# Kernel optimization log

Measured on AMD Instinct MI355X. Metric: run time of the kernel, lower is better.

The kernel has to match this reference:

```python
import jax, jax.numpy as jnp
import numpy as np

EMB_DIM = 1024
HEAD = 16
HEAD_DIM = EMB_DIM // HEAD


def setup_inputs() -> dict:
    key = jax.random.key(0)
    ks = jax.random.split(key, 6)
    s = 1.0 / np.sqrt(EMB_DIM)
    return {
        "z": jax.random.normal(ks[0], (4, 2048, EMB_DIM), dtype=jnp.float32),
        "w_q": jax.random.normal(ks[1], (EMB_DIM, EMB_DIM), dtype=jnp.float32) * s,
        "w_k": jax.random.normal(ks[2], (EMB_DIM, EMB_DIM), dtype=jnp.float32) * s,
        "w_v": jax.random.normal(ks[3], (EMB_DIM, EMB_DIM), dtype=jnp.float32) * s,
        "w_o": jax.random.normal(ks[4], (EMB_DIM, EMB_DIM), dtype=jnp.float32) * s,
        "b_o": jax.random.normal(ks[5], (EMB_DIM,), dtype=jnp.float32) * 0.01,
    }


def reference(z, w_q, w_k, w_v, w_o, b_o):
    B, N, D = z.shape
    # QKV projections (nn.Linear: x @ W.T; here weights stored as (D_in, D_out))
    q = (z @ w_q).reshape(B, N, HEAD, HEAD_DIM).transpose(0, 2, 1, 3)  # bhnd
    k = (z @ w_k).reshape(B, N, HEAD, HEAD_DIM).transpose(0, 2, 1, 3)
    v = (z @ w_v).reshape(B, N, HEAD, HEAD_DIM).transpose(0, 2, 1, 3)
    scale = 1.0 / np.sqrt(HEAD_DIM).astype(np.float32)
    dots = jnp.einsum("bhnd,bhmd->bhnm", q, k) * scale
    attn = jax.nn.softmax(dots, axis=-1)
    out = jnp.einsum("bhnm,bhmd->bhnd", attn, v)
    out = out.transpose(0, 2, 1, 3).reshape(B, N, D)
    return out @ w_o + b_o
```

## Files before the change

### kernel.cpp

```cpp
#include <hip/hip_runtime.h>
#include <hip/hip_bf16.h>
#include <stdint.h>

typedef unsigned short u16;
typedef __attribute__((ext_vector_type(8))) short bf16x8;
typedef __attribute__((ext_vector_type(4))) float f32x4;
typedef __attribute__((ext_vector_type(16))) float f32x16;

static __device__ inline u16 f2bf(float f) {
  union { float f; uint32_t u; } v; v.f = f;
  uint32_t u = v.u;
  u += 0x7fffu + ((u >> 16) & 1);
  return (u16)(u >> 16);
}

static __device__ inline float fast_exp2(float x) {
#if __has_builtin(__builtin_amdgcn_exp2f)
  return __builtin_amdgcn_exp2f(x);
#else
  return __expf(x * 0.6931471805599453f);
#endif
}

static __device__ inline uint32_t pack_bf16(float lo, float hi) {
#if __has_builtin(__builtin_amdgcn_cvt_pk_bf16_f32)
  typedef __attribute__((ext_vector_type(2))) __bf16 bf16x2_t;
  bf16x2_t r = __builtin_amdgcn_cvt_pk_bf16_f32(lo, hi);
  union { bf16x2_t v; uint32_t u; } c; c.v = r;
  return c.u;
#else
  union { float f; uint32_t u; } a, b;
  a.f = lo; b.f = hi;
  uint32_t ua = a.u + 0x8000u;
  uint32_t ub = b.u + 0x8000u;
  return __builtin_amdgcn_perm(ub, ua, 0x07060302u);
#endif
}

__global__ __launch_bounds__(256) void cast_bf16_kernel(const float* __restrict__ src,
                                                        u16* __restrict__ dst, int n4) {
  int i = blockIdx.x * 256 + threadIdx.x;
  if (i < n4) {
    float4 v = reinterpret_cast<const float4*>(src)[i];
    uint2 o;
    o.x = (uint32_t)f2bf(v.x) | ((uint32_t)f2bf(v.y) << 16);
    o.y = (uint32_t)f2bf(v.z) | ((uint32_t)f2bf(v.w) << 16);
    reinterpret_cast<uint2*>(dst)[i] = o;
  }
}

__global__ __launch_bounds__(256) void wtrans_kernel(const float* __restrict__ wq,
                                                     const float* __restrict__ wk,
                                                     const float* __restrict__ wv,
                                                     const float* __restrict__ wo,
                                                     u16* __restrict__ bqkv,
                                                     u16* __restrict__ wot) {
  int z = blockIdx.z;
  const float* src = (z == 0) ? wq : (z == 1) ? wk : (z == 2) ? wv : wo;
  u16* dst = (z < 3) ? (bqkv + (size_t)z * 1024 * 1024) : wot;
  __shared__ float tile[32][33];
  int c0 = blockIdx.x * 32, r0 = blockIdx.y * 32;
  int tx = threadIdx.x, ty = threadIdx.y;
#pragma unroll
  for (int i = 0; i < 32; i += 8)
    tile[ty + i][tx] = src[(size_t)(r0 + ty + i) * 1024 + c0 + tx];
  __syncthreads();
#pragma unroll
  for (int i = 0; i < 32; i += 8)
    dst[(size_t)(c0 + ty + i) * 1024 + r0 + tx] = f2bf(tile[tx][ty + i]);
}

template <int MODE>
__global__ __launch_bounds__(256) void gemm_bt_kernel(
    const u16* __restrict__ A, const u16* __restrict__ Bt,
    u16* __restrict__ outQ, u16* __restrict__ outK, u16* __restrict__ outVt,
    float* __restrict__ outC, const float* __restrict__ bias) {
  const int Kd = 1024;
  const int n0 = blockIdx.x * 128;
  const int m0 = blockIdx.y * 128;
  __shared__ __align__(16) u16 Asm[128 * 40];
  __shared__ __align__(16) u16 Bsm[128 * 40];
  const int tid = threadIdx.x;
  const int wave = tid >> 6, lane = tid & 63;
  const int quad = lane >> 4, l15 = lane & 15;
  const int wm = (wave >> 1) * 64, wn = (wave & 1) * 64;
  const int srow = tid >> 2, spart = tid & 3;

  f32x4 acc[4][4] = {};

  for (int k0 = 0; k0 < Kd; k0 += 32) {
    __syncthreads();
    uint4 a0 = *reinterpret_cast<const uint4*>(A + (size_t)(m0 + srow) * Kd + k0 + spart * 8);
    uint4 a1 = *reinterpret_cast<const uint4*>(A + (size_t)(m0 + srow + 64) * Kd + k0 + spart * 8);
    uint4 b0 = *reinterpret_cast<const uint4*>(Bt + (size_t)(n0 + srow) * Kd + k0 + spart * 8);
    uint4 b1 = *reinterpret_cast<const uint4*>(Bt + (size_t)(n0 + srow + 64) * Kd + k0 + spart * 8);
    *reinterpret_cast<uint4*>(Asm + srow * 40 + spart * 8) = a0;
    *reinterpret_cast<uint4*>(Asm + (srow + 64) * 40 + spart * 8) = a1;
    *reinterpret_cast<uint4*>(Bsm + srow * 40 + spart * 8) = b0;
    *reinterpret_cast<uint4*>(Bsm + (srow + 64) * 40 + spart * 8) = b1;
    __syncthreads();
    bf16x8 af[4], bf[4];
#pragma unroll
    for (int i = 0; i < 4; i++)
      af[i] = *reinterpret_cast<const bf16x8*>(Asm + (wm + i * 16 + l15) * 40 + quad * 8);
#pragma unroll
    for (int i = 0; i < 4; i++)
      bf[i] = *reinterpret_cast<const bf16x8*>(Bsm + (wn + i * 16 + l15) * 40 + quad * 8);
#pragma unroll
    for (int mi = 0; mi < 4; mi++)
#pragma unroll
      for (int ni = 0; ni < 4; ni++)
        acc[mi][ni] = __builtin_amdgcn_mfma_f32_16x16x32_bf16(af[mi], bf[ni], acc[mi][ni], 0, 0, 0);
  }

  if (MODE == 0) {
    const int which = (n0 + wn) >> 10;
#pragma unroll
    for (int mi = 0; mi < 4; mi++)
#pragma unroll
      for (int ni = 0; ni < 4; ni++) {
        int n = n0 + wn + ni * 16 + l15;
        int hn = n & 1023;
        int h = hn >> 6, dim = hn & 63;
        if (which == 2) {
          int m = m0 + wm + mi * 16 + quad * 4;
          int b = m >> 11, tok = m & 2047;
          uint2 pk;
          pk.x = pack_bf16(acc[mi][ni][0], acc[mi][ni][1]);
          pk.y = pack_bf16(acc[mi][ni][2], acc[mi][ni][3]);
          *reinterpret_cast<uint2*>(outVt + ((size_t)(b * 16 + h) * 64 + dim) * 2048 + tok) = pk;
        } else {
          u16* dst = (which == 0) ? outQ : outK;
          float qscale = (which == 0) ? 0.1803368801111204f : 1.0f;
#pragma unroll
          for (int r = 0; r < 4; r++) {
            int m = m0 + wm + mi * 16 + quad * 4 + r;
            int b = m >> 11, tok = m & 2047;
            dst[(((size_t)(b * 16 + h)) * 2048 + tok) * 64 + dim] = f2bf(acc[mi][ni][r] * qscale);
          }
        }
      }
  } else {
#pragma unroll
    for (int mi = 0; mi < 4; mi++)
#pragma unroll
      for (int ni = 0; ni < 4; ni++) {
        int n = n0 + wn + ni * 16 + l15;
        float bv = bias[n];
#pragma unroll
        for (int r = 0; r < 4; r++) {
          int m = m0 + wm + mi * 16 + quad * 4 + r;
          outC[(size_t)m * 1024 + n] = acc[mi][ni][r] + bv;
        }
      }
  }
}

__global__ __launch_bounds__(256, 4) void attn_kernel(const u16* __restrict__ Q,
                                                      const u16* __restrict__ K,
                                                      const u16* __restrict__ Vt,
                                                      u16* __restrict__ Oout) {
  const int bh = blockIdx.y;
  const int q0 = blockIdx.x * 128;
  const int tid = threadIdx.x;
  const int wave = tid >> 6, lane = tid & 63;
  const int l31 = lane & 31, h = lane >> 5;

  __shared__ __align__(16) u16 QPs[128 * 72];
  __shared__ __align__(16) u16 Ks[64 * 72];
  __shared__ __align__(16) u16 Vs[64 * 72];

  const u16* Qg = Q + ((size_t)bh * 2048 + q0) * 64;
  const u16* Kg = K + (size_t)bh * 2048 * 64;
  const u16* Vg = Vt + (size_t)bh * 64 * 2048;

#pragma unroll
  for (int k = 0; k < 4; k++) {
    int c = tid + k * 256;
    int row = c >> 3, col = (c & 7) * 8;
    *reinterpret_cast<uint4*>(&QPs[row * 72 + col]) =
        *reinterpret_cast<const uint4*>(Qg + row * 64 + col);
  }
  __syncthreads();
  bf16x8 qf[4];
#pragma unroll
  for (int dc = 0; dc < 4; dc++)
    qf[dc] = *reinterpret_cast<const bf16x8*>(&QPs[(wave * 32 + l31) * 72 + dc * 16 + h * 8]);

  u16* Pw = &QPs[wave * 32 * 72];
  float ls0 = 0.f, ls1 = 0.f, ls2 = 0.f, ls3 = 0.f;
  f32x16 oacc[2] = {};

  for (int kt = 0; kt < 2048; kt += 64) {
    __syncthreads();
#pragma unroll
    for (int k = 0; k < 2; k++) {
      int c = tid + k * 256;
      int row = c >> 3, col = (c & 7) * 8;
      *reinterpret_cast<uint4*>(&Ks[row * 72 + col]) =
          *reinterpret_cast<const uint4*>(Kg + (size_t)(kt + row) * 64 + col);
      *reinterpret_cast<uint4*>(&Vs[row * 72 + col]) =
          *reinterpret_cast<const uint4*>(Vg + (size_t)row * 2048 + kt + col);
    }
    __syncthreads();

#pragma unroll
    for (int kb = 0; kb < 2; kb++) {
      f32x16 s = {};
#pragma unroll
      for (int dc = 0; dc < 4; dc++) {
        bf16x8 kf = *reinterpret_cast<const bf16x8*>(&Ks[(kb * 32 + l31) * 72 + dc * 16 + h * 8]);
        s = __builtin_amdgcn_mfma_f32_32x32x16_bf16(kf, qf[dc], s, 0, 0, 0);
      }
      float p[16];
#pragma unroll
      for (int i = 0; i < 16; i++) p[i] = fast_exp2(s[i]);
#pragma unroll
      for (int i = 0; i < 16; i += 4) {
        ls0 += p[i]; ls1 += p[i + 1]; ls2 += p[i + 2]; ls3 += p[i + 3];
      }
#pragma unroll
      for (int rg = 0; rg < 4; rg++) {
        uint2 pk;
        pk.x = pack_bf16(p[rg * 4 + 0], p[rg * 4 + 1]);
        pk.y = pack_bf16(p[rg * 4 + 2], p[rg * 4 + 3]);
        *reinterpret_cast<uint2*>(&Pw[l31 * 72 + kb * 32 + rg * 8 + h * 4]) = pk;
      }
    }

    bf16x8 pf[4];
#pragma unroll
    for (int kc = 0; kc < 4; kc++)
      pf[kc] = *reinterpret_cast<const bf16x8*>(&Pw[l31 * 72 + kc * 16 + h * 8]);
#pragma unroll
    for (int dt = 0; dt < 2; dt++) {
#pragma unroll
      for (int kc = 0; kc < 4; kc++) {
        bf16x8 vf = *reinterpret_cast<const bf16x8*>(&Vs[(dt * 32 + l31) * 72 + kc * 16 + h * 8]);
        oacc[dt] = __builtin_amdgcn_mfma_f32_32x32x16_bf16(pf[kc], vf, oacc[dt], 0, 0, 0);
      }
    }
  }

  float lsum = (ls0 + ls1) + (ls2 + ls3);
  lsum += __shfl_xor(lsum, 32, 64);
  float inv[16];
#pragma unroll
  for (int reg = 0; reg < 16; reg++) {
    int qq = (reg & 3) + 8 * (reg >> 2) + 4 * h;
    int lv = __builtin_amdgcn_ds_bpermute(qq << 2, __float_as_int(lsum));
    inv[reg] = __builtin_amdgcn_rcpf(__int_as_float(lv));
  }

  const int b = bh >> 4, hd = bh & 15;
  u16* dst = Oout + (size_t)b * 2048 * 1024 + (size_t)hd * 64;
#pragma unroll
  for (int dt = 0; dt < 2; dt++)
#pragma unroll
    for (int reg = 0; reg < 16; reg++) {
      int qq = q0 + wave * 32 + (reg & 3) + 8 * (reg >> 2) + 4 * h;
      dst[(size_t)qq * 1024 + dt * 32 + l31] = f2bf(oacc[dt][reg] * inv[reg]);
    }
}

extern "C" void kernel_launch(void* const* d_in, const int* in_sizes, int n_in,
                              void* d_out, int out_size, void* d_ws, size_t ws_size,
                              hipStream_t stream) {
  (void)in_sizes; (void)n_in; (void)out_size; (void)ws_size;
  const float* z  = (const float*)d_in[0];
  const float* wq = (const float*)d_in[1];
  const float* wk = (const float*)d_in[2];
  const float* wv = (const float*)d_in[3];
  const float* wo = (const float*)d_in[4];
  const float* bo = (const float*)d_in[5];
  float* out = (float*)d_out;

  char* ws = (char*)d_ws;
  u16* zb   = (u16*)(ws);
  u16* bqkv = (u16*)(ws + (16ull << 20));
  u16* wot  = (u16*)(ws + (22ull << 20));
  u16* Qb   = (u16*)(ws + (24ull << 20));
  u16* Kb   = (u16*)(ws + (40ull << 20));
  u16* Vtb  = (u16*)(ws + (56ull << 20));
  u16* Ob   = zb;

  cast_bf16_kernel<<<8192, 256, 0, stream>>>(z, zb, 2097152);
  wtrans_kernel<<<dim3(32, 32, 4), dim3(32, 8), 0, stream>>>(wq, wk, wv, wo, bqkv, wot);
  gemm_bt_kernel<0><<<dim3(24, 64), 256, 0, stream>>>(zb, bqkv, Qb, Kb, Vtb, nullptr, nullptr);
  attn_kernel<<<dim3(16, 64), 256, 0, stream>>>(Qb, Kb, Vtb, Ob);
  gemm_bt_kernel<1><<<dim3(8, 64), 256, 0, stream>>>(Ob, wot, nullptr, nullptr, nullptr, out, bo);
}
```

Before: 308.1 us.

## Prefetch K/V tiles in registers, use direct global-to-LDS loads in GEMM

The attention kernel now loads the next K/V tile into registers while the current tile is being computed, then writes it to shared memory after a barrier. This hides global load latency behind the QK and PV MFMA work. The GEMM staging loads switch to global_load_lds with an unpadded 32-wide LDS layout, which may bring back bank conflicts on fragment reads. The attention grid is also swapped so that blocks sharing the same head launch apart, and the cast kernel now uses the packed bf16 conversion.

```diff
diff --git a/kernel.cpp b/kernel.cpp
--- a/kernel.cpp
+++ b/kernel.cpp
@@ -37,14 +37,20 @@
 #endif
 }
 
+static __device__ __forceinline__ void load_lds_128(const u16* g, u16* l) {
+  __builtin_amdgcn_global_load_lds((const __attribute__((address_space(1))) void*)g,
+                                   (__attribute__((address_space(3))) void*)l,
+                                   16, 0, 0);
+}
+
 __global__ __launch_bounds__(256) void cast_bf16_kernel(const float* __restrict__ src,
                                                         u16* __restrict__ dst, int n4) {
   int i = blockIdx.x * 256 + threadIdx.x;
   if (i < n4) {
     float4 v = reinterpret_cast<const float4*>(src)[i];
     uint2 o;
-    o.x = (uint32_t)f2bf(v.x) | ((uint32_t)f2bf(v.y) << 16);
-    o.y = (uint32_t)f2bf(v.z) | ((uint32_t)f2bf(v.w) << 16);
+    o.x = pack_bf16(v.x, v.y);
+    o.y = pack_bf16(v.z, v.w);
     reinterpret_cast<uint2*>(dst)[i] = o;
   }
 }
@@ -78,34 +84,37 @@
   const int Kd = 1024;
   const int n0 = blockIdx.x * 128;
   const int m0 = blockIdx.y * 128;
-  __shared__ __align__(16) u16 Asm[128 * 40];
-  __shared__ __align__(16) u16 Bsm[128 * 40];
+  __shared__ __align__(16) u16 Asm[128 * 32];
+  __shared__ __align__(16) u16 Bsm[128 * 32];
   const int tid = threadIdx.x;
   const int wave = tid >> 6, lane = tid & 63;
   const int quad = lane >> 4, l15 = lane & 15;
   const int wm = (wave >> 1) * 64, wn = (wave & 1) * 64;
-  const int srow = tid >> 2, spart = tid & 3;
+
+  const int c0 = wave * 128 + lane;
+  const int c1 = c0 + 64;
+  const int r0 = c0 >> 2, p0 = (c0 & 3) * 8;
+  const int r1 = c1 >> 2, p1 = (c1 & 3) * 8;
+
+  const u16* Ab = A + (size_t)m0 * Kd;
+  const u16* Bb = Bt + (size_t)n0 * Kd;
 
   f32x4 acc[4][4] = {};
 
   for (int k0 = 0; k0 < Kd; k0 += 32) {
     __syncthreads();
-    uint4 a0 = *reinterpret_cast<const uint4*>(A + (size_t)(m0 + srow) * Kd + k0 + spart * 8);
-    uint4 a1 = *reinterpret_cast<const uint4*>(A + (size_t)(m0 + srow + 64) * Kd + k0 + spart * 8);
-    uint4 b0 = *reinterpret_cast<const uint4*>(Bt + (size_t)(n0 + srow) * Kd + k0 + spart * 8);
-    uint4 b1 = *reinterpret_cast<const uint4*>(Bt + (size_t)(n0 + srow + 64) * Kd + k0 + spart * 8);
-    *reinterpret_cast<uint4*>(Asm + srow * 40 + spart * 8) = a0;
-    *reinterpret_cast<uint4*>(Asm + (srow + 64) * 40 + spart * 8) = a1;
-    *reinterpret_cast<uint4*>(Bsm + srow * 40 + spart * 8) = b0;
-    *reinterpret_cast<uint4*>(Bsm + (srow + 64) * 40 + spart * 8) = b1;
+    load_lds_128(Ab + (size_t)r0 * Kd + k0 + p0, Asm + c0 * 8);
+    load_lds_128(Ab + (size_t)r1 * Kd + k0 + p1, Asm + c1 * 8);
+    load_lds_128(Bb + (size_t)r0 * Kd + k0 + p0, Bsm + c0 * 8);
+    load_lds_128(Bb + (size_t)r1 * Kd + k0 + p1, Bsm + c1 * 8);
     __syncthreads();
     bf16x8 af[4], bf[4];
 #pragma unroll
     for (int i = 0; i < 4; i++)
-      af[i] = *reinterpret_cast<const bf16x8*>(Asm + (wm + i * 16 + l15) * 40 + quad * 8);
+      af[i] = *reinterpret_cast<const bf16x8*>(Asm + (wm + i * 16 + l15) * 32 + quad * 8);
 #pragma unroll
     for (int i = 0; i < 4; i++)
-      bf[i] = *reinterpret_cast<const bf16x8*>(Bsm + (wn + i * 16 + l15) * 40 + quad * 8);
+      bf[i] = *reinterpret_cast<const bf16x8*>(Bsm + (wn + i * 16 + l15) * 32 + quad * 8);
 #pragma unroll
     for (int mi = 0; mi < 4; mi++)
 #pragma unroll
@@ -160,8 +169,8 @@
                                                       const u16* __restrict__ K,
                                                       const u16* __restrict__ Vt,
                                                       u16* __restrict__ Oout) {
-  const int bh = blockIdx.y;
-  const int q0 = blockIdx.x * 128;
+  const int bh = blockIdx.x;
+  const int q0 = blockIdx.y * 128;
   const int tid = threadIdx.x;
   const int wave = tid >> 6, lane = tid & 63;
   const int l31 = lane & 31, h = lane >> 5;
@@ -181,28 +190,39 @@
     *reinterpret_cast<uint4*>(&QPs[row * 72 + col]) =
         *reinterpret_cast<const uint4*>(Qg + row * 64 + col);
   }
+
+  const int srow0 = tid >> 3, scol0 = (tid & 7) * 8;
+  const int srow1 = (tid + 256) >> 3, scol1 = scol0;
+
+  uint4 pk0 = *reinterpret_cast<const uint4*>(Kg + (size_t)srow0 * 64 + scol0);
+  uint4 pk1 = *reinterpret_cast<const uint4*>(Kg + (size_t)srow1 * 64 + scol1);
+  uint4 pv0 = *reinterpret_cast<const uint4*>(Vg + (size_t)srow0 * 2048 + scol0);
+  uint4 pv1 = *reinterpret_cast<const uint4*>(Vg + (size_t)srow1 * 2048 + scol1);
+
   __syncthreads();
   bf16x8 qf[4];
 #pragma unroll
   for (int dc = 0; dc < 4; dc++)
     qf[dc] = *reinterpret_cast<const bf16x8*>(&QPs[(wave * 32 + l31) * 72 + dc * 16 + h * 8]);
+
+  *reinterpret_cast<uint4*>(&Ks[srow0 * 72 + scol0]) = pk0;
+  *reinterpret_cast<uint4*>(&Ks[srow1 * 72 + scol1]) = pk1;
+  *reinterpret_cast<uint4*>(&Vs[srow0 * 72 + scol0]) = pv0;
+  *reinterpret_cast<uint4*>(&Vs[srow1 * 72 + scol1]) = pv1;
+  __syncthreads();
 
   u16* Pw = &QPs[wave * 32 * 72];
   float ls0 = 0.f, ls1 = 0.f, ls2 = 0.f, ls3 = 0.f;
   f32x16 oacc[2] = {};
 
   for (int kt = 0; kt < 2048; kt += 64) {
-    __syncthreads();
-#pragma unroll
-    for (int k = 0; k < 2; k++) {
-      int c = tid + k * 256;
-      int row = c >> 3, col = (c & 7) * 8;
-      *reinterpret_cast<uint4*>(&Ks[row * 72 + col]) =
-          *reinterpret_cast<const uint4*>(Kg + (size_t)(kt + row) * 64 + col);
-      *reinterpret_cast<uint4*>(&Vs[row * 72 + col]) =
-          *reinterpret_cast<const uint4*>(Vg + (size_t)row * 2048 + kt + col);
-    }
-    __syncthreads();
+    const bool pf = (kt + 64) < 2048;
+    if (pf) {
+      pk0 = *reinterpret_cast<const uint4*>(Kg + (size_t)(kt + 64 + srow0) * 64 + scol0);
+      pk1 = *reinterpret_cast<const uint4*>(Kg + (size_t)(kt + 64 + srow1) * 64 + scol1);
+      pv0 = *reinterpret_cast<const uint4*>(Vg + (size_t)srow0 * 2048 + kt + 64 + scol0);
+      pv1 = *reinterpret_cast<const uint4*>(Vg + (size_t)srow1 * 2048 + kt + 64 + scol1);
+    }
 
 #pragma unroll
     for (int kb = 0; kb < 2; kb++) {
@@ -228,18 +248,27 @@
       }
     }
 
-    bf16x8 pf[4];
+    bf16x8 pfr[4];
 #pragma unroll
     for (int kc = 0; kc < 4; kc++)
-      pf[kc] = *reinterpret_cast<const bf16x8*>(&Pw[l31 * 72 + kc * 16 + h * 8]);
+      pfr[kc] = *reinterpret_cast<const bf16x8*>(&Pw[l31 * 72 + kc * 16 + h * 8]);
 #pragma unroll
     for (int dt = 0; dt < 2; dt++) {
 #pragma unroll
       for (int kc = 0; kc < 4; kc++) {
         bf16x8 vf = *reinterpret_cast<const bf16x8*>(&Vs[(dt * 32 + l31) * 72 + kc * 16 + h * 8]);
-        oacc[dt] = __builtin_amdgcn_mfma_f32_32x32x16_bf16(pf[kc], vf, oacc[dt], 0, 0, 0);
-      }
-    }
+        oacc[dt] = __builtin_amdgcn_mfma_f32_32x32x16_bf16(pfr[kc], vf, oacc[dt], 0, 0, 0);
+      }
+    }
+
+    __syncthreads();
+    if (pf) {
+      *reinterpret_cast<uint4*>(&Ks[srow0 * 72 + scol0]) = pk0;
+      *reinterpret_cast<uint4*>(&Ks[srow1 * 72 + scol1]) = pk1;
+      *reinterpret_cast<uint4*>(&Vs[srow0 * 72 + scol0]) = pv0;
+      *reinterpret_cast<uint4*>(&Vs[srow1 * 72 + scol1]) = pv1;
+    }
+    __syncthreads();
   }
 
   float lsum = (ls0 + ls1) + (ls2 + ls3);
@@ -287,6 +316,6 @@
   cast_bf16_kernel<<<8192, 256, 0, stream>>>(z, zb, 2097152);
   wtrans_kernel<<<dim3(32, 32, 4), dim3(32, 8), 0, stream>>>(wq, wk, wv, wo, bqkv, wot);
   gemm_bt_kernel<0><<<dim3(24, 64), 256, 0, stream>>>(zb, bqkv, Qb, Kb, Vtb, nullptr, nullptr);
-  attn_kernel<<<dim3(16, 64), 256, 0, stream>>>(Qb, Kb, Vtb, Ob);
+  attn_kernel<<<dim3(64, 16), 256, 0, stream>>>(Qb, Kb, Vtb, Ob);
   gemm_bt_kernel<1><<<dim3(8, 64), 256, 0, stream>>>(Ob, wot, nullptr, nullptr, nullptr, out, bo);
 }
```

Measured after the change: 324.5 us. +5.3%, slower.
